# Performance work log

Measured on AMD Instinct MI355X. Metric: run time of the kernel, lower is better.

## Reference

```python
import jax, jax.numpy as jnp
import numpy as np

DIMS = [30, 64, 32, 16, 8, 2]

def _kaiming_uniform(key, fan_out, fan_in):
    # torch kaiming_uniform_ default: a=0 -> gain=sqrt(2), bound=gain*sqrt(3/fan_in)
    bound = np.sqrt(2.0) * np.sqrt(3.0 / fan_in)
    return jax.random.uniform(key, (fan_out, fan_in), jnp.float32, -bound, bound)

def setup_inputs() -> dict:
    key = jax.random.key(0)
    ks = jax.random.split(key, 6)
    inp = {"x": jax.random.normal(ks[0], (1000000, DIMS[0]), jnp.float32)}
    for i in range(5):
        inp[f"w{i+1}"] = _kaiming_uniform(ks[i + 1], DIMS[i + 1], DIMS[i])
        inp[f"b{i+1}"] = jnp.zeros((DIMS[i + 1],), jnp.float32)
    return inp

def reference(x, w1, b1, w2, b2, w3, b3, w4, b4, w5, b5):
    # quant/dequant stubs are identity in fp32 mode
    h = jax.nn.relu(x @ w1.T + b1)
    h = jax.nn.relu(h @ w2.T + b2)
    h = jax.nn.relu(h @ w3.T + b3)
    h = jax.nn.relu(h @ w4.T + b4)
    return h @ w5.T + b5
```

## Files before the change

kernel.cpp:

```cpp
#include <hip/hip_runtime.h>
#include <hip/hip_bf16.h>


typedef float        f32x4 __attribute__((ext_vector_type(4)));
typedef unsigned int u32x4 __attribute__((ext_vector_type(4)));
typedef short        s16x8 __attribute__((ext_vector_type(8)));

static __device__ __forceinline__ unsigned int pkbf(float a, float b) {
    unsigned int ua = __builtin_bit_cast(unsigned int, a) + 0x8000u;
    unsigned int ub = __builtin_bit_cast(unsigned int, b) + 0x8000u;
    return __builtin_amdgcn_perm(ub, ua, 0x07060302u);
}
static __device__ __forceinline__ unsigned int rp2(float a, float b) {
    return pkbf(fmaxf(a, 0.0f), fmaxf(b, 0.0f));
}
static __device__ __forceinline__ unsigned short f2bf(float f) {
    __hip_bfloat16 h = __float2bfloat16(f);
    unsigned short r;
    __builtin_memcpy(&r, &h, sizeof(r));
    return r;
}

static __device__ __forceinline__ void gld16(const void* g, void* l) {
    __builtin_amdgcn_global_load_lds(
        (const __attribute__((address_space(1))) unsigned int*)g,
        (__attribute__((address_space(3))) unsigned int*)l, 16, 0, 0);
}
static __device__ __forceinline__ void gld4(const void* g, void* l) {
    __builtin_amdgcn_global_load_lds(
        (const __attribute__((address_space(1))) unsigned int*)g,
        (__attribute__((address_space(3))) unsigned int*)l, 4, 0, 0);
}

#define MFMA(A, B, C) __builtin_amdgcn_mfma_f32_16x16x32_bf16((A), (B), (C), 0, 0, 0)

#define SLOT_B 4096
#define NSLOT  2

__global__ __launch_bounds__(256) void mlp_mfma_kernel(
    const float* __restrict__ x,
    const float* __restrict__ w1, const float* __restrict__ b1,
    const float* __restrict__ w2, const float* __restrict__ b2,
    const float* __restrict__ w3, const float* __restrict__ b3,
    const float* __restrict__ w4, const float* __restrict__ b4,
    const float* __restrict__ w5, const float* __restrict__ b5,
    float* __restrict__ out, int n)
{
    __shared__ __attribute__((aligned(16))) unsigned char ldsX[4][NSLOT * SLOT_B];

    const int lane = threadIdx.x & 63;
    const int wv   = threadIdx.x >> 6;
    const int g    = lane >> 4;
    const int ml   = lane & 15;

    unsigned char* myL = &ldsX[wv][0];

    #pragma unroll
    for (int s = 0; s < NSLOT; ++s)
        *(unsigned int*)(myL + s * SLOT_B + 3840 + lane * 4) = 0u;

    s16x8 A1[4], A2[2][2], A3, A4, A5;
    #pragma unroll
    for (int t = 0; t < 4; ++t) {
        #pragma unroll
        for (int i = 0; i < 8; ++i) {
            const int k = 4*g + (i & 3) + ((i >> 2) << 4);
            const int m = 16*t + ml;
            float v = (k < 30) ? w1[m*30 + k] : 0.0f;
            A1[t][i] = (short)f2bf(v);
        }
    }
    #pragma unroll
    for (int t = 0; t < 2; ++t)
        #pragma unroll
        for (int s = 0; s < 2; ++s)
            #pragma unroll
            for (int i = 0; i < 8; ++i) {
                const int k = 4*g + (i & 3) + ((i >> 2) << 4);
                A2[t][s][i] = (short)f2bf(w2[(16*t + ml)*64 + 32*s + k]);
            }
    #pragma unroll
    for (int i = 0; i < 8; ++i) {
        const int k = 4*g + (i & 3) + ((i >> 2) << 4);
        A3[i] = (short)f2bf(w3[ml*32 + k]);
        float v4 = 0.0f, v5 = 0.0f;
        if (ml < 8) v4 = (k < 16) ? w4[ml*16 + k] : ((k == 16) ? b4[ml] : 0.0f);
        if (ml < 2) v5 = (k <  8) ? w5[ml*8  + k] : ((k ==  8) ? b5[ml] : 0.0f);
        A4[i] = (short)f2bf(v4);
        A5[i] = (short)f2bf(v5);
    }
    f32x4 bias1[4], bias2[2], bias3;
    #pragma unroll
    for (int t = 0; t < 4; ++t)
        #pragma unroll
        for (int q = 0; q < 4; ++q)
            bias1[t][q] = b1[16*t + 4*g + q];
    #pragma unroll
    for (int t = 0; t < 2; ++t)
        #pragma unroll
        for (int q = 0; q < 4; ++q)
            bias2[t][q] = b2[16*t + 4*g + q];
    #pragma unroll
    for (int q = 0; q < 4; ++q)
        bias3[q] = b3[4*g + q];

    const int ntiles = (n + 15) >> 4;
    const int npairs = (ntiles + 1) >> 1;
    const int NW = gridDim.x * 4;
    const int p0 = blockIdx.x * 4 + wv;
    if (p0 >= npairs) return;

    const size_t xbytes = (size_t)n * 120;

    auto issue = [&](int pr, int sl) {
        size_t gb = (size_t)pr * 3840;
        if (gb + 3840 > xbytes) gb = xbytes - 3840;
        const unsigned char* gp = (const unsigned char*)x + gb;
        unsigned char* lp = myL + sl * SLOT_B;
        gld16(gp +        (size_t)lane * 16, lp);
        gld16(gp + 1024 + (size_t)lane * 16, lp + 1024);
        gld16(gp + 2048 + (size_t)lane * 16, lp + 2048);
        gld4 (gp + 3072 + (size_t)lane * 4,  lp + 3072);
        gld4 (gp + 3328 + (size_t)lane * 4,  lp + 3328);
        gld4 (gp + 3584 + (size_t)lane * 4,  lp + 3584);
    };

    issue(p0, 0);

    const f32x4 zero = {0.0f, 0.0f, 0.0f, 0.0f};
    int slot = 0;

    for (int p = p0; p < npairs; p += NW) {
        if (p + NW < npairs) {
            issue(p + NW, slot ^ 1);
            asm volatile("s_waitcnt vmcnt(6)" ::: "memory");
        } else {
            asm volatile("s_waitcnt vmcnt(0)" ::: "memory");
        }

        s16x8 B0[2];
        const bool fullpair = ((p + 1) * 32 <= n);
        if (fullpair) {
            const float* L = (const float*)(myL + slot * SLOT_B);
            #pragma unroll
            for (int j = 0; j < 2; ++j) {
                const float* rp = L + (16*j + ml) * 30 + 4*g;
                float2 a01 = *(const float2*)(rp);
                float2 a23 = *(const float2*)(rp + 2);
                float2 b01 = *(const float2*)(rp + 16);
                float2 b23 = *(const float2*)(rp + 18);
                u32x4 u;
                u.x = pkbf(a01.x, a01.y); u.y = pkbf(a23.x, a23.y);
                u.z = pkbf(b01.x, b01.y); u.w = pkbf(b23.x, b23.y);
                B0[j] = __builtin_bit_cast(s16x8, u);
            }
        } else {
            #pragma unroll
            for (int j = 0; j < 2; ++j) {
                int row = p*32 + 16*j + ml;
                if (row >= n) row = n - 1;
                const float* rp = x + (size_t)row * 30 + 4*g;
                float2 a01 = *(const float2*)(rp);
                float2 a23 = *(const float2*)(rp + 2);
                float2 b01 = *(const float2*)(rp + 16);
                float2 b23 = (g < 3) ? *(const float2*)(rp + 18) : make_float2(0.f, 0.f);
                u32x4 u;
                u.x = pkbf(a01.x, a01.y); u.y = pkbf(a23.x, a23.y);
                u.z = pkbf(b01.x, b01.y); u.w = pkbf(b23.x, b23.y);
                B0[j] = __builtin_bit_cast(s16x8, u);
            }
        }

        f32x4 c1[2][4];
        #pragma unroll
        for (int t = 0; t < 4; ++t)
            #pragma unroll
            for (int j = 0; j < 2; ++j)
                c1[j][t] = MFMA(A1[t], B0[j], bias1[t]);

        s16x8 B1[2][2];
        #pragma unroll
        for (int j = 0; j < 2; ++j)
            #pragma unroll
            for (int s = 0; s < 2; ++s) {
                u32x4 u;
                u.x = rp2(c1[j][2*s][0],     c1[j][2*s][1]);
                u.y = rp2(c1[j][2*s][2],     c1[j][2*s][3]);
                u.z = rp2(c1[j][2*s + 1][0], c1[j][2*s + 1][1]);
                u.w = rp2(c1[j][2*s + 1][2], c1[j][2*s + 1][3]);
                B1[j][s] = __builtin_bit_cast(s16x8, u);
            }
        f32x4 c2[2][2];
        #pragma unroll
        for (int t = 0; t < 2; ++t)
            #pragma unroll
            for (int j = 0; j < 2; ++j) {
                f32x4 a = bias2[t];
                #pragma unroll
                for (int s = 0; s < 2; ++s) a = MFMA(A2[t][s], B1[j][s], a);
                c2[j][t] = a;
            }

        f32x4 c3[2];
        #pragma unroll
        for (int j = 0; j < 2; ++j) {
            u32x4 u2;
            u2.x = rp2(c2[j][0][0], c2[j][0][1]);
            u2.y = rp2(c2[j][0][2], c2[j][0][3]);
            u2.z = rp2(c2[j][1][0], c2[j][1][1]);
            u2.w = rp2(c2[j][1][2], c2[j][1][3]);
            c3[j] = MFMA(A3, __builtin_bit_cast(s16x8, u2), bias3);
        }

        f32x4 c4[2];
        #pragma unroll
        for (int j = 0; j < 2; ++j) {
            u32x4 u3;
            u3.x = rp2(c3[j][0], c3[j][1]);
            u3.y = rp2(c3[j][2], c3[j][3]);
            u3.z = (g == 0) ? 0x3F80u : 0u;
            u3.w = 0u;
            c4[j] = MFMA(A4, __builtin_bit_cast(s16x8, u3), zero);
        }

        f32x4 c5[2];
        #pragma unroll
        for (int j = 0; j < 2; ++j) {
            u32x4 u4;
            u4.x = (g == 2) ? 0x3F80u : rp2(c4[j][0], c4[j][1]);
            u4.y = (g == 2) ? 0u      : rp2(c4[j][2], c4[j][3]);
            u4.z = 0u; u4.w = 0u;
            c5[j] = MFMA(A5, __builtin_bit_cast(s16x8, u4), zero);
        }

        #pragma unroll
        for (int j = 0; j < 2; ++j) {
            const int orow = (2*p + j)*16 + lane;
            if (lane < 16 && orow < n) {
                float2 o; o.x = c5[j][0]; o.y = c5[j][1];
                *(float2*)(out + (size_t)orow * 2) = o;
            }
        }

        slot ^= 1;
    }
}

extern "C" void kernel_launch(void* const* d_in, const int* in_sizes, int n_in,
                              void* d_out, int out_size, void* d_ws, size_t ws_size,
                              hipStream_t stream) {
    const float* x  = (const float*)d_in[0];
    const float* w1 = (const float*)d_in[1];
    const float* b1 = (const float*)d_in[2];
    const float* w2 = (const float*)d_in[3];
    const float* b2 = (const float*)d_in[4];
    const float* w3 = (const float*)d_in[5];
    const float* b3 = (const float*)d_in[6];
    const float* w4 = (const float*)d_in[7];
    const float* b4 = (const float*)d_in[8];
    const float* w5 = (const float*)d_in[9];
    const float* b5 = (const float*)d_in[10];
    float* out = (float*)d_out;

    const int n = in_sizes[0] / 30;
    const int ntiles = (n + 15) >> 4;
    const int npairs = (ntiles + 1) >> 1;
    int blocks = (npairs + 3) / 4;
    if (blocks > 1280) blocks = 1280;

    mlp_mfma_kernel<<<blocks, 256, 0, stream>>>(
        x, w1, b1, w2, b2, w3, b3, w4, b4, w5, b5, out, n);
}
```

Baseline: 43.33 us.

## Prefetch next x tile into registers instead of async global-to-LDS double buffer

```diff
diff --git a/kernel.cpp b/kernel.cpp
--- a/kernel.cpp
+++ b/kernel.cpp
@@ -21,21 +21,9 @@
     return r;
 }
 
-static __device__ __forceinline__ void gld16(const void* g, void* l) {
-    __builtin_amdgcn_global_load_lds(
-        (const __attribute__((address_space(1))) unsigned int*)g,
-        (__attribute__((address_space(3))) unsigned int*)l, 16, 0, 0);
-}
-static __device__ __forceinline__ void gld4(const void* g, void* l) {
-    __builtin_amdgcn_global_load_lds(
-        (const __attribute__((address_space(1))) unsigned int*)g,
-        (__attribute__((address_space(3))) unsigned int*)l, 4, 0, 0);
-}
-
 #define MFMA(A, B, C) __builtin_amdgcn_mfma_f32_16x16x32_bf16((A), (B), (C), 0, 0, 0)
 
-#define SLOT_B 4096
-#define NSLOT  2
+#define SLOT_B 4352
 
 __global__ __launch_bounds__(256) void mlp_mfma_kernel(
     const float* __restrict__ x,
@@ -46,7 +34,7 @@
     const float* __restrict__ w5, const float* __restrict__ b5,
     float* __restrict__ out, int n)
 {
-    __shared__ __attribute__((aligned(16))) unsigned char ldsX[4][NSLOT * SLOT_B];
+    __shared__ __attribute__((aligned(16))) unsigned char ldsX[4][SLOT_B];
 
     const int lane = threadIdx.x & 63;
     const int wv   = threadIdx.x >> 6;
@@ -55,9 +43,7 @@
 
     unsigned char* myL = &ldsX[wv][0];
 
-    #pragma unroll
-    for (int s = 0; s < NSLOT; ++s)
-        *(unsigned int*)(myL + s * SLOT_B + 3840 + lane * 4) = 0u;
+    *(unsigned int*)(myL + 4096 + lane * 4) = 0u;
 
     s16x8 A1[4], A2[2][2], A3, A4, A5;
     #pragma unroll
@@ -112,36 +98,36 @@
 
     const size_t xbytes = (size_t)n * 120;
 
-    auto issue = [&](int pr, int sl) {
+    auto loadpair = [&](int pr, f32x4 r[4], int& delta) {
         size_t gb = (size_t)pr * 3840;
-        if (gb + 3840 > xbytes) gb = xbytes - 3840;
-        const unsigned char* gp = (const unsigned char*)x + gb;
-        unsigned char* lp = myL + sl * SLOT_B;
-        gld16(gp +        (size_t)lane * 16, lp);
-        gld16(gp + 1024 + (size_t)lane * 16, lp + 1024);
-        gld16(gp + 2048 + (size_t)lane * 16, lp + 2048);
-        gld4 (gp + 3072 + (size_t)lane * 4,  lp + 3072);
-        gld4 (gp + 3328 + (size_t)lane * 4,  lp + 3328);
-        gld4 (gp + 3584 + (size_t)lane * 4,  lp + 3584);
+        if (gb + 4096 > xbytes) gb = xbytes - 4096;
+        delta = (int)((size_t)pr * 3840 - gb);
+        const unsigned char* gp = (const unsigned char*)x + gb + (size_t)lane * 16;
+        r[0] = *(const f32x4*)(gp);
+        r[1] = *(const f32x4*)(gp + 1024);
+        r[2] = *(const f32x4*)(gp + 2048);
+        r[3] = *(const f32x4*)(gp + 3072);
     };
 
-    issue(p0, 0);
+    f32x4 rA[4], rB[4];
+    int deltaA = 0, deltaB = 0;
+    loadpair(p0, rA, deltaA);
 
     const f32x4 zero = {0.0f, 0.0f, 0.0f, 0.0f};
-    int slot = 0;
 
     for (int p = p0; p < npairs; p += NW) {
-        if (p + NW < npairs) {
-            issue(p + NW, slot ^ 1);
-            asm volatile("s_waitcnt vmcnt(6)" ::: "memory");
-        } else {
-            asm volatile("s_waitcnt vmcnt(0)" ::: "memory");
+        {
+            unsigned char* lp = myL + lane * 16;
+            *(f32x4*)(lp)        = rA[0];
+            *(f32x4*)(lp + 1024) = rA[1];
+            *(f32x4*)(lp + 2048) = rA[2];
+            *(f32x4*)(lp + 3072) = rA[3];
         }
 
         s16x8 B0[2];
         const bool fullpair = ((p + 1) * 32 <= n);
         if (fullpair) {
-            const float* L = (const float*)(myL + slot * SLOT_B);
+            const float* L = (const float*)(myL + deltaA);
             #pragma unroll
             for (int j = 0; j < 2; ++j) {
                 const float* rp = L + (16*j + ml) * 30 + 4*g;
@@ -171,6 +157,9 @@
             }
         }
 
+        const int pn = p + NW;
+        if (pn < npairs) loadpair(pn, rB, deltaB);
+
         f32x4 c1[2][4];
         #pragma unroll
         for (int t = 0; t < 4; ++t)
@@ -242,7 +231,9 @@
             }
         }
 
-        slot ^= 1;
+        #pragma unroll
+        for (int q = 0; q < 4; ++q) rA[q] = rB[q];
+        deltaA = deltaB;
     }
 }
 
```

Result: faster. 41.36 us (median of 2 runs) (-4.5%).
